# Kernel optimization log

Measured on AMD Instinct MI355X. Metric: run time of the kernel, lower is better.

Reference implementation:

```python
import jax, jax.numpy as jnp
import numpy as np

D_MODEL = 2048
NUM_HEADS = 16
HEAD_DIM = D_MODEL // NUM_HEADS  # 128
BASE = 10000.0


def rotate_half(x):
    x1, x2 = x[..., : x.shape[-1] // 2], x[..., x.shape[-1] // 2 :]
    return jnp.concatenate((-x2, x1), axis=-1)


def setup_inputs() -> dict:
    key = jax.random.key(0)
    ks = jax.random.split(key, 9)
    B, S, D = 2, 2048, D_MODEL
    s = 1.0 / np.sqrt(D)
    return {
        "x": jax.random.normal(ks[0], (B, S, D), dtype=jnp.float32),
        "Wq": jax.random.normal(ks[1], (D, D), dtype=jnp.float32) * s,
        "bq": jnp.zeros((D,), dtype=jnp.float32),
        "Wk": jax.random.normal(ks[2], (D, D), dtype=jnp.float32) * s,
        "bk": jnp.zeros((D,), dtype=jnp.float32),
        "Wv": jax.random.normal(ks[3], (D, D), dtype=jnp.float32) * s,
        "bv": jnp.zeros((D,), dtype=jnp.float32),
        "Wo": jax.random.normal(ks[4], (D, D), dtype=jnp.float32) * s,
        "bo": jnp.zeros((D,), dtype=jnp.float32),
    }


def reference(x, Wq, bq, Wk, bk, Wv, bv, Wo, bo):
    B, S, D = x.shape
    H, hd = NUM_HEADS, HEAD_DIM

    def proj(W, b):
        # nn.Linear: x @ W^T + b, then split heads -> [B, H, S, hd]
        return (x @ W.T + b).reshape(B, S, H, hd).transpose(0, 2, 1, 3)

    q = proj(Wq, bq)
    k = proj(Wk, bk)
    v = proj(Wv, bv)

    # Rotary embedding table (note: original applies cos()/sin() to a
    # tensor that already contains [sin(si), cos(si)] — reproduced faithfully).
    positions = jnp.arange(S, dtype=jnp.float32)
    inv_freq = 1.0 / (BASE ** (jnp.arange(0, hd, 2, dtype=jnp.float32) / hd))
    sinusoid = positions[:, None] * inv_freq[None, :]            # [S, hd/2]
    emb = jnp.concatenate((jnp.sin(sinusoid), jnp.cos(sinusoid)), axis=-1)  # [S, hd]
    cos_e = jnp.cos(emb)  # broadcast over [B, H, S, hd]
    sin_e = jnp.sin(emb)

    q_rot = q * cos_e + rotate_half(q) * sin_e
    k_rot = k * cos_e + rotate_half(k) * sin_e

    scale = 1.0 / jnp.sqrt(jnp.asarray(hd, dtype=x.dtype))
    attn = jnp.einsum("bhqd,bhkd->bhqk", q_rot, k_rot) * scale
    attn = jax.nn.softmax(attn, axis=-1)
    out = jnp.einsum("bhqk,bhkd->bhqd", attn, v)
    out = out.transpose(0, 2, 1, 3).reshape(B, S, D)
    return out @ Wo.T + bo
```

## Files before the change

kernel.cpp:

```cpp
#include <hip/hip_runtime.h>
#include <math.h>

#define D_MODEL 2048
#define NHEADS  16
#define HD      128
#define SEQ     2048
#define BATCH   2
#define SCALE   0.08838834764831845f

typedef __attribute__((ext_vector_type(8))) short short8;
typedef __attribute__((ext_vector_type(4))) float f32x4;

#define MFMA16(a,b,c) __builtin_amdgcn_mfma_f32_16x16x32_bf16((a),(b),(c),0,0,0)

__device__ __forceinline__ unsigned short f2bf(float x){
    unsigned u = __float_as_uint(x);
    return (unsigned short)((u + 0x7FFFu + ((u>>16)&1u)) >> 16);
}
__device__ __forceinline__ float bf2f(unsigned short h){ return __uint_as_float(((unsigned)h)<<16); }

__device__ __forceinline__ void async16(void* lds, const void* g){
    __builtin_amdgcn_global_load_lds((const __attribute__((address_space(1))) unsigned int*)g,
                                     (__attribute__((address_space(3))) unsigned int*)lds, 16, 0, 0);
}

__global__ __launch_bounds__(256)
void split_w(const float* __restrict__ src, unsigned short* __restrict__ hi,
             unsigned short* __restrict__ lo, int n4, int write_lo)
{
    int i = blockIdx.x*256 + threadIdx.x;
    if (i >= n4) return;
    float4 v = ((const float4*)src)[i];
    ushort4 h, l;
    h.x=f2bf(v.x); l.x=f2bf(v.x-bf2f(h.x));
    h.y=f2bf(v.y); l.y=f2bf(v.y-bf2f(h.y));
    h.z=f2bf(v.z); l.z=f2bf(v.z-bf2f(h.z));
    h.w=f2bf(v.w); l.w=f2bf(v.w-bf2f(h.w));
    ((ushort4*)hi)[i]=h;
    if (write_lo) ((ushort4*)lo)[i]=l;
}

__global__ __launch_bounds__(256)
void rope_table(float4* __restrict__ tab)
{
    int i = blockIdx.x*256 + threadIdx.x;
    int s = i >> 6, d = i & 63;
    float f = powf(10000.0f, -(float)d * (1.0f/64.0f));
    float sv = (float)s * f;
    float sn = sinf(sv), cs = cosf(sv);
    tab[i] = (float4){cosf(sn), sinf(sn), cosf(cs), sinf(cs)};
}

__global__ __launch_bounds__(256,2)
void gemm_qkv(const float* __restrict__ x, const unsigned short* __restrict__ wsplit,
              const float* __restrict__ bq, const float* __restrict__ bk, const float* __restrict__ bv,
              const float4* __restrict__ tab,
              unsigned short* __restrict__ Qhi, unsigned short* __restrict__ Qlo,
              unsigned short* __restrict__ Khi, unsigned short* __restrict__ Klo,
              unsigned short* __restrict__ Vt)
{
    const int z = blockIdx.z;
    const unsigned short* Whi = wsplit + (size_t)z*8388608u;
    const unsigned short* Wlo = Whi + 4194304u;
    const float* bias = (z==0)?bq:((z==1)?bk:bv);

    const int t = threadIdx.x, w = t>>6, lane = t&63;
    const int quad = lane>>4, l15 = lane&15;
    const int mhalf = (w>>1)*64, nhalf = (w&1)*64;
    const int m0 = blockIdx.y*128, n0 = blockIdx.x*128;

    __shared__ __align__(16) unsigned short gsm[17408];
    unsigned short* Ahi = gsm;
    unsigned short* Alo = gsm + 4096;
    unsigned short* Bhi = gsm + 8192;
    unsigned short* Blo = gsm + 12288;

    f32x4 acc[4][4];
#pragma unroll
    for (int i=0;i<4;i++)
#pragma unroll
        for (int j=0;j<4;j++) acc[i][j] = (f32x4){0.f,0.f,0.f,0.f};

    for (int kt=0; kt<2048; kt+=32) {
        float4 xv[4];
#pragma unroll
        for (int i=0;i<4;i++){
            int idx=t+256*i; int row=idx>>3, seg=idx&7;
            xv[i] = *(const float4*)(x + (size_t)(m0+row)*2048 + kt + seg*4);
        }
        __syncthreads();
#pragma unroll
        for (int i=0;i<4;i++){
            int idx=t+256*i; int row=idx>>3, seg=idx&7;
            int sw = ((seg>>1) ^ ((row>>1)&3))*8 + (seg&1)*4;
            ushort4 h,l;
            h.x=f2bf(xv[i].x); l.x=f2bf(xv[i].x-bf2f(h.x));
            h.y=f2bf(xv[i].y); l.y=f2bf(xv[i].y-bf2f(h.y));
            h.z=f2bf(xv[i].z); l.z=f2bf(xv[i].z-bf2f(h.z));
            h.w=f2bf(xv[i].w); l.w=f2bf(xv[i].w-bf2f(h.w));
            *(ushort4*)&Ahi[row*32+sw] = h;
            *(ushort4*)&Alo[row*32+sw] = l;
        }
#pragma unroll
        for (int j=0;j<2;j++){
            int idx=t+256*j; int rw=idx>>2, sg=idx&3;
            int sgp = sg ^ ((rw>>1)&3);
            async16((char*)&Bhi[rw*32+sg*8], Whi + (size_t)(n0+rw)*2048 + kt + sgp*8);
            if (z != 2)
                async16((char*)&Blo[rw*32+sg*8], Wlo + (size_t)(n0+rw)*2048 + kt + sgp*8);
        }
        __syncthreads();

        short8 af_h[4], af_l[4], bf_h[4], bf_l[4];
#pragma unroll
        for (int mi=0;mi<4;mi++){
            int m = mhalf + mi*16 + l15;
            int c = (quad ^ ((m>>1)&3))*8;
            af_h[mi] = *(const short8*)&Ahi[m*32 + c];
            af_l[mi] = *(const short8*)&Alo[m*32 + c];
        }
#pragma unroll
        for (int ni=0;ni<4;ni++){
            int n = nhalf + ni*16 + l15;
            int c = (quad ^ ((n>>1)&3))*8;
            bf_h[ni] = *(const short8*)&Bhi[n*32 + c];
            bf_l[ni] = *(const short8*)&Blo[n*32 + c];
        }
#pragma unroll
        for (int mi=0;mi<4;mi++)
#pragma unroll
            for (int ni=0;ni<4;ni++){
                acc[mi][ni] = MFMA16(af_h[mi], bf_h[ni], acc[mi][ni]);
                acc[mi][ni] = MFMA16(af_l[mi], bf_h[ni], acc[mi][ni]);
                if (z != 2) acc[mi][ni] = MFMA16(af_h[mi], bf_l[ni], acc[mi][ni]);
            }
    }
    __syncthreads();

#pragma unroll
    for (int ni=0;ni<4;ni++){
        float bv_ = bias[n0 + nhalf + ni*16 + l15];
#pragma unroll
        for (int mi=0;mi<4;mi++){
            acc[mi][ni][0]+=bv_; acc[mi][ni][1]+=bv_; acc[mi][ni][2]+=bv_; acc[mi][ni][3]+=bv_;
        }
    }

    const int h = blockIdx.x;
    if (z == 2) {
#pragma unroll
        for (int mi=0;mi<4;mi++)
#pragma unroll
        for (int ni=0;ni<4;ni++)
#pragma unroll
        for (int r=0;r<4;r++){
            int d = nhalf + ni*16 + l15;
            int ml = mhalf + mi*16 + quad*4 + r;
            gsm[d*136 + ml] = f2bf(acc[mi][ni][r]);
        }
        __syncthreads();
        const int b = m0>>11, s0 = m0&2047;
        unsigned short* vdst = Vt + ((size_t)(b*16+h)*128)*2048;
        const int dr = t>>1, half = (t&1)*64;
#pragma unroll
        for (int j=0;j<8;j++){
            uint4 v = *(const uint4*)&gsm[dr*136 + half + j*8];
            *(uint4*)(vdst + (size_t)dr*2048 + s0 + half + j*8) = v;
        }
    } else {
        float* xch = (float*)gsm;
        if (w & 1) {
#pragma unroll
            for (int mi=0;mi<4;mi++)
#pragma unroll
            for (int ni=0;ni<4;ni++)
#pragma unroll
            for (int r=0;r<4;r++)
                xch[(mhalf+mi*16+quad*4+r)*64 + ni*16+l15] = acc[mi][ni][r];
        }
        __syncthreads();
        if (!(w & 1)) {
            unsigned short* OHi = (z==0)?Qhi:Khi;
            unsigned short* OLo = (z==0)?Qlo:Klo;
            const float scl = (z==0)?SCALE:1.0f;
#pragma unroll
            for (int ni=0;ni<4;ni++){
                int d = ni*16 + l15;
                for (int mi=0;mi<4;mi++)
                for (int r=0;r<4;r++){
                    int ml = mhalf + mi*16 + quad*4 + r;
                    int mg = m0 + ml;
                    int b = mg>>11, s = mg&2047;
                    float4 tv = tab[s*64 + d];
                    float c_lo = acc[mi][ni][r];
                    float c_hi = xch[ml*64 + d];
                    float o1 = (c_lo*tv.x - c_hi*tv.y)*scl;
                    float o2 = (c_hi*tv.z + c_lo*tv.w)*scl;
                    size_t base = ((size_t)(b*16+h)*2048 + s)*128;
                    unsigned short h1=f2bf(o1); OHi[base+d]=h1;    OLo[base+d]=f2bf(o1-bf2f(h1));
                    unsigned short h2=f2bf(o2); OHi[base+64+d]=h2; OLo[base+64+d]=f2bf(o2-bf2f(h2));
                }
            }
        }
    }
}

__global__ __launch_bounds__(256,2)
void flash_mfma(const unsigned short* __restrict__ Qhi, const unsigned short* __restrict__ Qlo,
                const unsigned short* __restrict__ Khi, const unsigned short* __restrict__ Klo,
                const unsigned short* __restrict__ Vt,
                unsigned short* __restrict__ Ohi, unsigned short* __restrict__ Olo)
{
    const int t=threadIdx.x, w=t>>6, lane=t&63, quad=lane>>4, l15=lane&15;
    const int bh = blockIdx.y, qt = blockIdx.x;

    __shared__ __align__(16) unsigned short sm[32768];
    unsigned short* Ps = sm + 24576 + w*2048;

    short8 qf[2][2][4];
    const size_t qrow = (size_t)bh*2048 + qt*128 + w*32;
#pragma unroll
    for (int mb=0;mb<2;mb++){
        size_t r = qrow + mb*16 + l15;
#pragma unroll
        for (int kc=0;kc<4;kc++){
            qf[0][mb][kc] = *(const short8*)(Qhi + r*128 + kc*32 + quad*8);
            qf[1][mb][kc] = *(const short8*)(Qlo + r*128 + kc*32 + quad*8);
        }
    }

    f32x4 O[2][8];
#pragma unroll
    for (int mb=0;mb<2;mb++)
#pragma unroll
        for (int nb=0;nb<8;nb++) O[mb][nb]=(f32x4){0.f,0.f,0.f,0.f};
    float mrow[2][4], lrow[2][4];
#pragma unroll
    for (int mb=0;mb<2;mb++)
#pragma unroll
        for (int r=0;r<4;r++){ mrow[mb][r]=-INFINITY; lrow[mb][r]=0.f; }

    const char* KhiB = (const char*)(Khi + (size_t)bh*2048*128);
    const char* KloB = (const char*)(Klo + (size_t)bh*2048*128);
    const unsigned short* VtB = Vt + (size_t)bh*128*2048;
    char* smb = (char*)sm;

    for (int kt=0; kt<2048; kt+=64) {
#pragma unroll
        for (int i=0;i<4;i++){
            int o16 = t + 256*i;
            int krow = o16>>4, kc = o16&15;
            int kcp = kc ^ (krow&15);
            async16(smb + i*4096 + t*16,         KhiB + (size_t)kt*256 + krow*256 + kcp*16);
            async16(smb + 16384 + i*4096 + t*16, KloB + (size_t)kt*256 + krow*256 + kcp*16);
            int d = (t>>3) + i*32, c = t&7;
            int cp = c ^ (d&7);
            async16(smb + 32768 + i*4096 + t*16, VtB + (size_t)d*2048 + kt + cp*8);
        }
        __syncthreads();

        f32x4 S[2][4];
#pragma unroll
        for (int mb=0;mb<2;mb++)
#pragma unroll
            for (int nb=0;nb<4;nb++) S[mb][nb]=(f32x4){0.f,0.f,0.f,0.f};
#pragma unroll
        for (int kc=0;kc<4;kc++)
#pragma unroll
        for (int nb=0;nb<4;nb++){
            int m = nb*16+l15;
            int c = ((kc*4+quad) ^ (m&15))*8;
            short8 kh = *(const short8*)&sm[m*128 + c];
            short8 kl = *(const short8*)&sm[8192 + m*128 + c];
#pragma unroll
            for (int mb=0;mb<2;mb++){
                S[mb][nb] = MFMA16(qf[0][mb][kc], kh, S[mb][nb]);
                S[mb][nb] = MFMA16(qf[1][mb][kc], kh, S[mb][nb]);
                S[mb][nb] = MFMA16(qf[0][mb][kc], kl, S[mb][nb]);
            }
        }

#pragma unroll
        for (int mb=0;mb<2;mb++){
            float mx[4], al[4], sum[4];
#pragma unroll
            for (int r=0;r<4;r++){
                float v = S[mb][0][r];
                v = fmaxf(v, S[mb][1][r]); v = fmaxf(v, S[mb][2][r]); v = fmaxf(v, S[mb][3][r]);
                mx[r]=v;
            }
#pragma unroll
            for (int d=1;d<16;d<<=1)
#pragma unroll
                for (int r=0;r<4;r++) mx[r] = fmaxf(mx[r], __shfl_xor(mx[r], d));
#pragma unroll
            for (int r=0;r<4;r++){
                float mn = fmaxf(mrow[mb][r], mx[r]);
                al[r] = __expf(mrow[mb][r]-mn);
                mrow[mb][r]=mn; sum[r]=0.f;
            }
#pragma unroll
            for (int nb=0;nb<4;nb++)
#pragma unroll
            for (int r=0;r<4;r++){
                float p = __expf(S[mb][nb][r] - mrow[mb][r]);
                sum[r] += p;
                int q = mb*16 + quad*4 + r;
                int c = nb*16 + l15;
                Ps[q*64 + (((c>>3)^(q&7))<<3) + (c&7)] = f2bf(p);
            }
#pragma unroll
            for (int d=1;d<16;d<<=1)
#pragma unroll
                for (int r=0;r<4;r++) sum[r] += __shfl_xor(sum[r], d);
#pragma unroll
            for (int r=0;r<4;r++) lrow[mb][r] = lrow[mb][r]*al[r] + sum[r];
#pragma unroll
            for (int nb=0;nb<8;nb++){
                O[mb][nb][0]*=al[0]; O[mb][nb][1]*=al[1]; O[mb][nb][2]*=al[2]; O[mb][nb][3]*=al[3];
            }
        }

#pragma unroll
        for (int kc2=0;kc2<2;kc2++){
            short8 pf0 = *(const short8*)&Ps[(l15)*64      + (((kc2*4+quad)^(l15&7))<<3)];
            short8 pf1 = *(const short8*)&Ps[(16+l15)*64   + (((kc2*4+quad)^(l15&7))<<3)];
#pragma unroll
            for (int nb=0;nb<8;nb++){
                int d = nb*16+l15;
                int c = ((kc2*4+quad) ^ (d&7))*8;
                short8 vf = *(const short8*)&sm[16384 + d*64 + c];
                O[0][nb] = MFMA16(pf0, vf, O[0][nb]);
                O[1][nb] = MFMA16(pf1, vf, O[1][nb]);
            }
        }
        __syncthreads();
    }

    const int b = bh>>4, h = bh&15;
#pragma unroll
    for (int mb=0;mb<2;mb++)
#pragma unroll
    for (int nb=0;nb<8;nb++)
#pragma unroll
    for (int r=0;r<4;r++){
        float v = O[mb][nb][r] / lrow[mb][r];
        int qg = qt*128 + w*32 + mb*16 + quad*4 + r;
        size_t base = ((size_t)(b*2048 + qg))*2048 + h*128 + nb*16 + l15;
        unsigned short hh = f2bf(v);
        Ohi[base]=hh; Olo[base]=f2bf(v-bf2f(hh));
    }
}

__global__ __launch_bounds__(256,2)
void gemm_out(const unsigned short* __restrict__ Ahi_g, const unsigned short* __restrict__ Alo_g,
              const unsigned short* __restrict__ Whi_g, const unsigned short* __restrict__ Wlo_g,
              const float* __restrict__ bias, float* __restrict__ out)
{
    const int t = threadIdx.x, w = t>>6, lane = t&63;
    const int quad = lane>>4, l15 = lane&15;
    const int mhalf = (w>>1)*64, nhalf = (w&1)*64;
    const int m0 = blockIdx.y*128, n0 = blockIdx.x*128;

    __shared__ __align__(16) unsigned short gsm[16384];
    unsigned short* Ahi = gsm;
    unsigned short* Alo = gsm + 4096;
    unsigned short* Bhi = gsm + 8192;
    unsigned short* Blo = gsm + 12288;

    f32x4 acc[4][4];
#pragma unroll
    for (int i=0;i<4;i++)
#pragma unroll
        for (int j=0;j<4;j++) acc[i][j] = (f32x4){0.f,0.f,0.f,0.f};

    for (int kt=0; kt<2048; kt+=32) {
        __syncthreads();
#pragma unroll
        for (int j=0;j<2;j++){
            int idx=t+256*j; int rw=idx>>2, sg=idx&3;
            int sgp = sg ^ ((rw>>1)&3);
            async16((char*)&Ahi[rw*32+sg*8], Ahi_g + (size_t)(m0+rw)*2048 + kt + sgp*8);
            async16((char*)&Alo[rw*32+sg*8], Alo_g + (size_t)(m0+rw)*2048 + kt + sgp*8);
            async16((char*)&Bhi[rw*32+sg*8], Whi_g + (size_t)(n0+rw)*2048 + kt + sgp*8);
            async16((char*)&Blo[rw*32+sg*8], Wlo_g + (size_t)(n0+rw)*2048 + kt + sgp*8);
        }
        __syncthreads();

        short8 af_h[4], af_l[4], bf_h[4], bf_l[4];
#pragma unroll
        for (int mi=0;mi<4;mi++){
            int m = mhalf + mi*16 + l15;
            int c = (quad ^ ((m>>1)&3))*8;
            af_h[mi] = *(const short8*)&Ahi[m*32 + c];
            af_l[mi] = *(const short8*)&Alo[m*32 + c];
        }
#pragma unroll
        for (int ni=0;ni<4;ni++){
            int n = nhalf + ni*16 + l15;
            int c = (quad ^ ((n>>1)&3))*8;
            bf_h[ni] = *(const short8*)&Bhi[n*32 + c];
            bf_l[ni] = *(const short8*)&Blo[n*32 + c];
        }
#pragma unroll
        for (int mi=0;mi<4;mi++)
#pragma unroll
            for (int ni=0;ni<4;ni++){
                acc[mi][ni] = MFMA16(af_h[mi], bf_h[ni], acc[mi][ni]);
                acc[mi][ni] = MFMA16(af_l[mi], bf_h[ni], acc[mi][ni]);
                acc[mi][ni] = MFMA16(af_h[mi], bf_l[ni], acc[mi][ni]);
            }
    }

#pragma unroll
    for (int ni=0;ni<4;ni++){
        int n = n0 + nhalf + ni*16 + l15;
        float bv_ = bias[n];
#pragma unroll
        for (int mi=0;mi<4;mi++)
#pragma unroll
        for (int r=0;r<4;r++){
            int m = m0 + mhalf + mi*16 + quad*4 + r;
            out[(size_t)m*2048 + n] = acc[mi][ni][r] + bv_;
        }
    }
}

extern "C" void kernel_launch(void* const* d_in, const int* in_sizes, int n_in,
                              void* d_out, int out_size, void* d_ws, size_t ws_size,
                              hipStream_t stream)
{
    (void)in_sizes; (void)n_in; (void)out_size; (void)ws_size;
    const float* x  = (const float*)d_in[0];
    const float* Wq = (const float*)d_in[1];
    const float* bq = (const float*)d_in[2];
    const float* Wk = (const float*)d_in[3];
    const float* bk = (const float*)d_in[4];
    const float* Wv = (const float*)d_in[5];
    const float* bv = (const float*)d_in[6];
    const float* Wo = (const float*)d_in[7];
    const float* bo = (const float*)d_in[8];
    float* out = (float*)d_out;

    unsigned short* wsB = (unsigned short*)d_ws;
    unsigned short* C0  = wsB + 20971520u;
    unsigned short* Qhi = C0;
    unsigned short* Qlo = C0 + 8388608u;
    unsigned short* Khi = C0 + 16777216u;
    unsigned short* Klo = C0 + 25165824u;
    unsigned short* Vt  = C0 + 33554432u;
    float4* tab = (float4*)(wsB + 62914560u);

    split_w<<<4096,256,0,stream>>>(Wq, wsB,            wsB+4194304u,  1048576, 1);
    split_w<<<4096,256,0,stream>>>(Wk, wsB+8388608u,   wsB+12582912u, 1048576, 1);
    split_w<<<4096,256,0,stream>>>(Wv, wsB+16777216u,  wsB+16777216u, 1048576, 0);
    rope_table<<<512,256,0,stream>>>(tab);

    gemm_qkv<<<dim3(16,32,3),256,0,stream>>>(x, wsB, bq,bk,bv, tab, Qhi,Qlo,Khi,Klo,Vt);

    unsigned short* Ohi = wsB;
    unsigned short* Olo = wsB + 8388608u;
    flash_mfma<<<dim3(16,32),256,0,stream>>>(Qhi,Qlo,Khi,Klo,Vt, Ohi, Olo);

    unsigned short* WoHi = C0;
    unsigned short* WoLo = C0 + 4194304u;
    split_w<<<4096,256,0,stream>>>(Wo, WoHi, WoLo, 1048576, 1);

    gemm_out<<<dim3(16,32),256,0,stream>>>(Ohi, Olo, WoHi, WoLo, bo, out);
}
```

Baseline: 769.9 us.

## Pre-split x into bf16 hi/lo and load A tiles asynchronously into LDS

Adds a split_w pass that converts x into bf16 hi/lo halves once, stored in the output buffer as scratch. gemm_qkv then loads A tiles with async global-to-LDS copies instead of per-tile fp32 loads, register conversion and LDS stores, which removes redundant conversion across the 16 column blocks and register pressure. The RoPE epilogue now shares its work across all four waves through a padded exchange buffer, where before half the waves sat idle. Launch bounds are raised to 3 blocks per SM for both GEMMs, and Blo loads are skipped for V. The trade-off is an extra kernel and extra global traffic for the split x.

```diff
diff --git a/kernel.cpp b/kernel.cpp
--- a/kernel.cpp
+++ b/kernel.cpp
@@ -51,8 +51,9 @@
     tab[i] = (float4){cosf(sn), sinf(sn), cosf(cs), sinf(cs)};
 }
 
-__global__ __launch_bounds__(256,2)
-void gemm_qkv(const float* __restrict__ x, const unsigned short* __restrict__ wsplit,
+__global__ __launch_bounds__(256,3)
+void gemm_qkv(const unsigned short* __restrict__ Xhi_g, const unsigned short* __restrict__ Xlo_g,
+              const unsigned short* __restrict__ wsplit,
               const float* __restrict__ bq, const float* __restrict__ bk, const float* __restrict__ bv,
               const float4* __restrict__ tab,
               unsigned short* __restrict__ Qhi, unsigned short* __restrict__ Qlo,
@@ -82,32 +83,18 @@
         for (int j=0;j<4;j++) acc[i][j] = (f32x4){0.f,0.f,0.f,0.f};
 
     for (int kt=0; kt<2048; kt+=32) {
-        float4 xv[4];
-#pragma unroll
-        for (int i=0;i<4;i++){
-            int idx=t+256*i; int row=idx>>3, seg=idx&7;
-            xv[i] = *(const float4*)(x + (size_t)(m0+row)*2048 + kt + seg*4);
-        }
-        __syncthreads();
-#pragma unroll
-        for (int i=0;i<4;i++){
-            int idx=t+256*i; int row=idx>>3, seg=idx&7;
-            int sw = ((seg>>1) ^ ((row>>1)&3))*8 + (seg&1)*4;
-            ushort4 h,l;
-            h.x=f2bf(xv[i].x); l.x=f2bf(xv[i].x-bf2f(h.x));
-            h.y=f2bf(xv[i].y); l.y=f2bf(xv[i].y-bf2f(h.y));
-            h.z=f2bf(xv[i].z); l.z=f2bf(xv[i].z-bf2f(h.z));
-            h.w=f2bf(xv[i].w); l.w=f2bf(xv[i].w-bf2f(h.w));
-            *(ushort4*)&Ahi[row*32+sw] = h;
-            *(ushort4*)&Alo[row*32+sw] = l;
-        }
+        __syncthreads();
 #pragma unroll
         for (int j=0;j<2;j++){
             int idx=t+256*j; int rw=idx>>2, sg=idx&3;
             int sgp = sg ^ ((rw>>1)&3);
-            async16((char*)&Bhi[rw*32+sg*8], Whi + (size_t)(n0+rw)*2048 + kt + sgp*8);
+            size_t goffA = (size_t)(m0+rw)*2048 + kt + sgp*8;
+            size_t goffB = (size_t)(n0+rw)*2048 + kt + sgp*8;
+            async16((char*)&Ahi[rw*32+sg*8], Xhi_g + goffA);
+            async16((char*)&Alo[rw*32+sg*8], Xlo_g + goffA);
+            async16((char*)&Bhi[rw*32+sg*8], Whi + goffB);
             if (z != 2)
-                async16((char*)&Blo[rw*32+sg*8], Wlo + (size_t)(n0+rw)*2048 + kt + sgp*8);
+                async16((char*)&Blo[rw*32+sg*8], Wlo + goffB);
         }
         __syncthreads();
 
@@ -124,7 +111,7 @@
             int n = nhalf + ni*16 + l15;
             int c = (quad ^ ((n>>1)&3))*8;
             bf_h[ni] = *(const short8*)&Bhi[n*32 + c];
-            bf_l[ni] = *(const short8*)&Blo[n*32 + c];
+            if (z != 2) bf_l[ni] = *(const short8*)&Blo[n*32 + c];
         }
 #pragma unroll
         for (int mi=0;mi<4;mi++)
@@ -169,37 +156,47 @@
         }
     } else {
         float* xch = (float*)gsm;
-        if (w & 1) {
+        if (!(w & 1)) {
 #pragma unroll
             for (int mi=0;mi<4;mi++)
 #pragma unroll
-            for (int ni=0;ni<4;ni++)
+            for (int ni=2;ni<4;ni++)
 #pragma unroll
             for (int r=0;r<4;r++)
-                xch[(mhalf+mi*16+quad*4+r)*64 + ni*16+l15] = acc[mi][ni][r];
-        }
-        __syncthreads();
-        if (!(w & 1)) {
-            unsigned short* OHi = (z==0)?Qhi:Khi;
-            unsigned short* OLo = (z==0)?Qlo:Klo;
-            const float scl = (z==0)?SCALE:1.0f;
-#pragma unroll
-            for (int ni=0;ni<4;ni++){
-                int d = ni*16 + l15;
-                for (int mi=0;mi<4;mi++)
-                for (int r=0;r<4;r++){
-                    int ml = mhalf + mi*16 + quad*4 + r;
-                    int mg = m0 + ml;
-                    int b = mg>>11, s = mg&2047;
-                    float4 tv = tab[s*64 + d];
-                    float c_lo = acc[mi][ni][r];
-                    float c_hi = xch[ml*64 + d];
-                    float o1 = (c_lo*tv.x - c_hi*tv.y)*scl;
-                    float o2 = (c_hi*tv.z + c_lo*tv.w)*scl;
-                    size_t base = ((size_t)(b*16+h)*2048 + s)*128;
-                    unsigned short h1=f2bf(o1); OHi[base+d]=h1;    OLo[base+d]=f2bf(o1-bf2f(h1));
-                    unsigned short h2=f2bf(o2); OHi[base+64+d]=h2; OLo[base+64+d]=f2bf(o2-bf2f(h2));
-                }
+                xch[(mhalf+mi*16+quad*4+r)*68 + (ni-2)*16+l15] = acc[mi][ni][r];
+        } else {
+#pragma unroll
+            for (int mi=0;mi<4;mi++)
+#pragma unroll
+            for (int ni=0;ni<2;ni++)
+#pragma unroll
+            for (int r=0;r<4;r++)
+                xch[(mhalf+mi*16+quad*4+r)*68 + 32 + ni*16+l15] = acc[mi][ni][r];
+        }
+        __syncthreads();
+        unsigned short* OHi = (z==0)?Qhi:Khi;
+        unsigned short* OLo = (z==0)?Qlo:Klo;
+        const float scl = (z==0)?SCALE:1.0f;
+        const int odd = w & 1;
+#pragma unroll
+        for (int ni2=0;ni2<2;ni2++){
+            int ni = odd ? (ni2+2) : ni2;
+            int d  = odd ? (32 + ni2*16 + l15) : (ni2*16 + l15);
+#pragma unroll
+            for (int mi=0;mi<4;mi++)
+#pragma unroll
+            for (int r=0;r<4;r++){
+                int ml = mhalf + mi*16 + quad*4 + r;
+                int mg = m0 + ml;
+                int b = mg>>11, s = mg&2047;
+                float4 tv = tab[s*64 + d];
+                float c_lo = odd ? xch[ml*68 + (d-32)] : acc[mi][ni][r];
+                float c_hi = odd ? acc[mi][ni][r]      : xch[ml*68 + 32 + d];
+                float o1 = (c_lo*tv.x - c_hi*tv.y)*scl;
+                float o2 = (c_hi*tv.z + c_lo*tv.w)*scl;
+                size_t base = ((size_t)(b*16+h)*2048 + s)*128;
+                unsigned short h1=f2bf(o1); OHi[base+d]=h1;    OLo[base+d]=f2bf(o1-bf2f(h1));
+                unsigned short h2=f2bf(o2); OHi[base+64+d]=h2; OLo[base+64+d]=f2bf(o2-bf2f(h2));
             }
         }
     }
@@ -352,7 +349,7 @@
     }
 }
 
-__global__ __launch_bounds__(256,2)
+__global__ __launch_bounds__(256,3)
 void gemm_out(const unsigned short* __restrict__ Ahi_g, const unsigned short* __restrict__ Alo_g,
               const unsigned short* __restrict__ Whi_g, const unsigned short* __restrict__ Wlo_g,
               const float* __restrict__ bias, float* __restrict__ out)
@@ -451,12 +448,17 @@
     unsigned short* Vt  = C0 + 33554432u;
     float4* tab = (float4*)(wsB + 62914560u);
 
+    unsigned short* Xhi = (unsigned short*)d_out;
+    unsigned short* Xlo = Xhi + 8388608u;
+
+    split_w<<<8192,256,0,stream>>>(x,  Xhi,            Xlo,           2097152, 1);
     split_w<<<4096,256,0,stream>>>(Wq, wsB,            wsB+4194304u,  1048576, 1);
     split_w<<<4096,256,0,stream>>>(Wk, wsB+8388608u,   wsB+12582912u, 1048576, 1);
     split_w<<<4096,256,0,stream>>>(Wv, wsB+16777216u,  wsB+16777216u, 1048576, 0);
     rope_table<<<512,256,0,stream>>>(tab);
 
-    gemm_qkv<<<dim3(16,32,3),256,0,stream>>>(x, wsB, bq,bk,bv, tab, Qhi,Qlo,Khi,Klo,Vt);
+    gemm_qkv<<<dim3(16,32,3),256,0,stream>>>(Xhi, Xlo, wsB, bq,bk,bv, tab,
+                                             Qhi,Qlo,Khi,Klo,Vt);
 
     unsigned short* Ohi = wsB;
     unsigned short* Olo = wsB + 8388608u;
```

Result: slower. 2.603 ms (+238.1%).
